# Optimization experiments

Measured on AMD Instinct MI355X. Metric: run time of the kernel, lower is better.

Reference implementation:

```python
import jax, jax.numpy as jnp
import numpy as np

H = 64  # hidden_size
IN = 1  # input_size
OUT = 32  # fc output


def _lstm_layer(x, Wih, Whh, bih, bhh):
    """x: (B,T,D_in). Returns (outputs (B,T,H), final h (B,H)). PyTorch gate order i,f,g,o."""
    B = x.shape[0]
    b = bih + bhh  # (4H,)
    # precompute input contributions for all timesteps: (T,B,4H)
    xW = jnp.einsum('btd,gd->tbg', x, Wih) + b

    def step(carry, xw_t):
        h, c = carry
        gates = xw_t + h @ Whh.T  # (B,4H)
        i, f, g, o = jnp.split(gates, 4, axis=-1)
        i = jax.nn.sigmoid(i)
        f = jax.nn.sigmoid(f)
        g = jnp.tanh(g)
        o = jax.nn.sigmoid(o)
        c = f * c + i * g
        h = o * jnp.tanh(c)
        return (h, c), h

    h0 = jnp.zeros((B, H), dtype=x.dtype)
    c0 = jnp.zeros((B, H), dtype=x.dtype)
    (h_T, _), hs = jax.lax.scan(step, (h0, c0), xW)
    return jnp.swapaxes(hs, 0, 1), h_T


def setup_inputs() -> dict:
    key = jax.random.key(0)
    ks = jax.random.split(key, 11)
    s_ih0 = 1.0 / np.sqrt(H)
    inp = {
        'x': jax.random.normal(ks[0], (2048, 512, IN), dtype=jnp.float32),
        # layer 0: input_size -> H
        'Wih0': jax.random.uniform(ks[1], (4 * H, IN), minval=-s_ih0, maxval=s_ih0),
        'Whh0': jax.random.uniform(ks[2], (4 * H, H), minval=-s_ih0, maxval=s_ih0),
        'bih0': jax.random.uniform(ks[3], (4 * H,), minval=-s_ih0, maxval=s_ih0),
        'bhh0': jax.random.uniform(ks[4], (4 * H,), minval=-s_ih0, maxval=s_ih0),
        # layer 1: H -> H
        'Wih1': jax.random.uniform(ks[5], (4 * H, H), minval=-s_ih0, maxval=s_ih0),
        'Whh1': jax.random.uniform(ks[6], (4 * H, H), minval=-s_ih0, maxval=s_ih0),
        'bih1': jax.random.uniform(ks[7], (4 * H,), minval=-s_ih0, maxval=s_ih0),
        'bhh1': jax.random.uniform(ks[8], (4 * H,), minval=-s_ih0, maxval=s_ih0),
        # fc: H -> 32
        'fcW': jax.random.uniform(ks[9], (OUT, H), minval=-s_ih0, maxval=s_ih0),
        'fcb': jax.random.uniform(ks[10], (OUT,), minval=-s_ih0, maxval=s_ih0),
    }
    return inp


def reference(x, Wih0, Whh0, bih0, bhh0, Wih1, Whh1, bih1, bhh1, fcW, fcb):
    h1_seq, _ = _lstm_layer(x, Wih0, Whh0, bih0, bhh0)
    _, h_last = _lstm_layer(h1_seq, Wih1, Whh1, bih1, bhh1)  # hidden[-1]
    features = jax.nn.relu(h_last @ fcW.T + fcb)  # (B, 32)
    return features
```

## Files before the change

kernel.cpp:

```cpp
#include <hip/hip_runtime.h>
#include <hip/hip_bf16.h>


#define HID 64
#define TSTEPS 512
#define MB 8
#define RS 80

typedef _Float16 f16x8 __attribute__((ext_vector_type(8)));
typedef float f32x4 __attribute__((ext_vector_type(4)));

#define KSIG (-1.44269504089f)
#define KTANH (2.88539008178f)

__device__ __forceinline__ float fsig(float x) {
    return __builtin_amdgcn_rcpf(1.f + __builtin_amdgcn_exp2f(KSIG * x));
}
__device__ __forceinline__ float ftanh(float x) {
    return 1.f - 2.f * __builtin_amdgcn_rcpf(1.f + __builtin_amdgcn_exp2f(KTANH * x));
}

__global__ __launch_bounds__(512, 1) void lstm_feat_kernel(
    const float* __restrict__ x,
    const float* __restrict__ Wih0, const float* __restrict__ Whh0,
    const float* __restrict__ bih0, const float* __restrict__ bhh0,
    const float* __restrict__ Wih1, const float* __restrict__ Whh1,
    const float* __restrict__ bih1, const float* __restrict__ bhh1,
    const float* __restrict__ fcW, const float* __restrict__ fcb,
    float* __restrict__ out)
{
    __shared__ float x_lds[TSTEPS * MB];
    __shared__ __align__(16) _Float16 h0_lds[2][MB * RS];
    __shared__ __align__(16) _Float16 h1_lds[2][MB * RS];
    __shared__ float h1f32[MB * HID];
    __shared__ float fcw_lds[HID * 32];
    __shared__ float fcb_lds[32];

    const int tid  = threadIdx.x;
    const int wave = tid >> 6;
    const int lane = tid & 63;
    const int nq   = lane & 15;
    const int quad = lane >> 4;
    const int bbase = blockIdx.x * MB;
    const bool isL1 = (wave >= 4);
    const int ug = wave & 3;
    const int u  = ug * 16 + nq;

    for (int i = tid; i < TSTEPS * MB; i += 512) {
        int r = i >> 9, t = i & (TSTEPS - 1);
        x_lds[t * MB + r] = x[(bbase + r) * TSTEPS + t];
    }
    for (int i = tid; i < 32 * HID; i += 512) {
        int o = i >> 6, kk = i & 63;
        fcw_lds[kk * 32 + o] = fcW[i];
    }
    if (tid < 32) fcb_lds[tid] = fcb[tid];
    for (int i = tid; i < 2 * MB * RS; i += 512) {
        ((_Float16*)h0_lds)[i] = (_Float16)0.f;
        ((_Float16*)h1_lds)[i] = (_Float16)0.f;
    }

    f16x8 wA[4][2], wB[4][2];
    float bA[4], wx0[4];
    {
        const float* Wa = isL1 ? Wih1 : Whh0;
        const float* Wb = isL1 ? Whh1 : Whh0;
        const float* bi = isL1 ? bih1 : bih0;
        const float* bh = isL1 ? bhh1 : bhh0;
        #pragma unroll
        for (int g = 0; g < 4; ++g) {
            const int n = g * 64 + u;
            bA[g]  = bi[n] + bh[n];
            wx0[g] = Wih0[n];
            #pragma unroll
            for (int ks = 0; ks < 2; ++ks) {
                const int k0 = quad * 8 + ks * 32;
                f16x8 a, b;
                #pragma unroll
                for (int j = 0; j < 8; ++j) {
                    a[j] = (_Float16)Wa[n * HID + k0 + j];
                    b[j] = (_Float16)Wb[n * HID + k0 + j];
                }
                wA[g][ks] = a; wB[g][ks] = b;
            }
        }
    }

    const f32x4 zero4 = {0.f, 0.f, 0.f, 0.f};
    const int arow = (nq >> 1) * RS + quad * 8;
    const int b0 = quad * 2;
    float c0 = 0.f, c1 = 0.f;

    __syncthreads();

    int p = 0;
    for (int k = 0; k < TSTEPS; ++k) {
        const int q = p ^ 1;
        if (!isL1) {
            f16x8 a0[2];
            a0[0] = *(const f16x8*)&h0_lds[p][arow];
            a0[1] = *(const f16x8*)&h0_lds[p][arow + 32];
            const float2 xq = *(const float2*)&x_lds[k * MB + b0];
            f32x4 acc[4];
            #pragma unroll
            for (int g = 0; g < 4; ++g)
                acc[g] = __builtin_amdgcn_mfma_f32_16x16x32_f16(a0[0], wA[g][0], zero4, 0, 0, 0);
            #pragma unroll
            for (int g = 0; g < 4; ++g)
                acc[g] = __builtin_amdgcn_mfma_f32_16x16x32_f16(a0[1], wA[g][1], acc[g], 0, 0, 0);
            {
                const float pi = acc[0][0] + fmaf(xq.x, wx0[0], bA[0]);
                const float pf = acc[1][0] + fmaf(xq.x, wx0[1], bA[1]);
                const float pg = acc[2][0] + fmaf(xq.x, wx0[2], bA[2]);
                const float po = acc[3][0] + fmaf(xq.x, wx0[3], bA[3]);
                const float iv = fsig(pi), fv = fsig(pf), gv = ftanh(pg), ov = fsig(po);
                c0 = fv * c0 + iv * gv;
                h0_lds[q][b0 * RS + u] = (_Float16)(ov * ftanh(c0));
            }
            {
                const float pi = acc[0][2] + fmaf(xq.y, wx0[0], bA[0]);
                const float pf = acc[1][2] + fmaf(xq.y, wx0[1], bA[1]);
                const float pg = acc[2][2] + fmaf(xq.y, wx0[2], bA[2]);
                const float po = acc[3][2] + fmaf(xq.y, wx0[3], bA[3]);
                const float iv = fsig(pi), fv = fsig(pf), gv = ftanh(pg), ov = fsig(po);
                c1 = fv * c1 + iv * gv;
                h0_lds[q][(b0 + 1) * RS + u] = (_Float16)(ov * ftanh(c1));
            }
        } else {
            f16x8 a0[2], a1[2];
            a0[0] = *(const f16x8*)&h0_lds[p][arow];
            a0[1] = *(const f16x8*)&h0_lds[p][arow + 32];
            a1[0] = *(const f16x8*)&h1_lds[p][arow];
            a1[1] = *(const f16x8*)&h1_lds[p][arow + 32];
            f32x4 accA[4], accB[4];
            #pragma unroll
            for (int g = 0; g < 4; ++g)
                accA[g] = __builtin_amdgcn_mfma_f32_16x16x32_f16(a0[0], wA[g][0], zero4, 0, 0, 0);
            #pragma unroll
            for (int g = 0; g < 4; ++g)
                accB[g] = __builtin_amdgcn_mfma_f32_16x16x32_f16(a1[0], wB[g][0], zero4, 0, 0, 0);
            #pragma unroll
            for (int g = 0; g < 4; ++g)
                accA[g] = __builtin_amdgcn_mfma_f32_16x16x32_f16(a0[1], wA[g][1], accA[g], 0, 0, 0);
            #pragma unroll
            for (int g = 0; g < 4; ++g)
                accB[g] = __builtin_amdgcn_mfma_f32_16x16x32_f16(a1[1], wB[g][1], accB[g], 0, 0, 0);
            if (k > 0) {
                {
                    const float pi = accA[0][0] + accB[0][0] + bA[0];
                    const float pf = accA[1][0] + accB[1][0] + bA[1];
                    const float pg = accA[2][0] + accB[2][0] + bA[2];
                    const float po = accA[3][0] + accB[3][0] + bA[3];
                    const float iv = fsig(pi), fv = fsig(pf), gv = ftanh(pg), ov = fsig(po);
                    c0 = fv * c0 + iv * gv;
                    h1_lds[q][b0 * RS + u] = (_Float16)(ov * ftanh(c0));
                }
                {
                    const float pi = accA[0][2] + accB[0][2] + bA[0];
                    const float pf = accA[1][2] + accB[1][2] + bA[1];
                    const float pg = accA[2][2] + accB[2][2] + bA[2];
                    const float po = accA[3][2] + accB[3][2] + bA[3];
                    const float iv = fsig(pi), fv = fsig(pf), gv = ftanh(pg), ov = fsig(po);
                    c1 = fv * c1 + iv * gv;
                    h1_lds[q][(b0 + 1) * RS + u] = (_Float16)(ov * ftanh(c1));
                }
            }
        }
        p = q;
        __syncthreads();
    }

    if (isL1) {
        f16x8 a0[2], a1[2];
        a0[0] = *(const f16x8*)&h0_lds[p][arow];
        a0[1] = *(const f16x8*)&h0_lds[p][arow + 32];
        a1[0] = *(const f16x8*)&h1_lds[p][arow];
        a1[1] = *(const f16x8*)&h1_lds[p][arow + 32];
        f32x4 accA[4], accB[4];
        #pragma unroll
        for (int g = 0; g < 4; ++g)
            accA[g] = __builtin_amdgcn_mfma_f32_16x16x32_f16(a0[0], wA[g][0], zero4, 0, 0, 0);
        #pragma unroll
        for (int g = 0; g < 4; ++g)
            accB[g] = __builtin_amdgcn_mfma_f32_16x16x32_f16(a1[0], wB[g][0], zero4, 0, 0, 0);
        #pragma unroll
        for (int g = 0; g < 4; ++g)
            accA[g] = __builtin_amdgcn_mfma_f32_16x16x32_f16(a0[1], wA[g][1], accA[g], 0, 0, 0);
        #pragma unroll
        for (int g = 0; g < 4; ++g)
            accB[g] = __builtin_amdgcn_mfma_f32_16x16x32_f16(a1[1], wB[g][1], accB[g], 0, 0, 0);
        {
            const float pi = accA[0][0] + accB[0][0] + bA[0];
            const float pf = accA[1][0] + accB[1][0] + bA[1];
            const float pg = accA[2][0] + accB[2][0] + bA[2];
            const float po = accA[3][0] + accB[3][0] + bA[3];
            const float iv = fsig(pi), fv = fsig(pf), gv = ftanh(pg), ov = fsig(po);
            c0 = fv * c0 + iv * gv;
            h1f32[b0 * HID + u] = ov * ftanh(c0);
        }
        {
            const float pi = accA[0][2] + accB[0][2] + bA[0];
            const float pf = accA[1][2] + accB[1][2] + bA[1];
            const float pg = accA[2][2] + accB[2][2] + bA[2];
            const float po = accA[3][2] + accB[3][2] + bA[3];
            const float iv = fsig(pi), fv = fsig(pf), gv = ftanh(pg), ov = fsig(po);
            c1 = fv * c1 + iv * gv;
            h1f32[(b0 + 1) * HID + u] = ov * ftanh(c1);
        }
    }
    __syncthreads();

    if (tid < MB * 32) {
        const int o  = tid & 31;
        const int rr = tid >> 5;
        float acc = fcb_lds[o];
        #pragma unroll 8
        for (int kk = 0; kk < HID; ++kk)
            acc += h1f32[rr * HID + kk] * fcw_lds[kk * 32 + o];
        out[(bbase + rr) * 32 + o] = fmaxf(acc, 0.f);
    }
}

extern "C" void kernel_launch(void* const* d_in, const int* in_sizes, int n_in,
                              void* d_out, int out_size, void* d_ws, size_t ws_size,
                              hipStream_t stream) {
    const float* x    = (const float*)d_in[0];
    const float* Wih0 = (const float*)d_in[1];
    const float* Whh0 = (const float*)d_in[2];
    const float* bih0 = (const float*)d_in[3];
    const float* bhh0 = (const float*)d_in[4];
    const float* Wih1 = (const float*)d_in[5];
    const float* Whh1 = (const float*)d_in[6];
    const float* bih1 = (const float*)d_in[7];
    const float* bhh1 = (const float*)d_in[8];
    const float* fcW  = (const float*)d_in[9];
    const float* fcb  = (const float*)d_in[10];
    float* out = (float*)d_out;

    lstm_feat_kernel<<<2048 / MB, 512, 0, stream>>>(
        x, Wih0, Whh0, bih0, bhh0, Wih1, Whh1, bih1, bhh1, fcW, fcb, out);
}
```

Measured before the change: 358.4 us.

## Fold activation scales and bias into MFMA, pack gate math as float2

Pre-scales the weights, biases and input weights by the sigmoid and tanh exp2 constants, so the activations skip a multiply. The bias now seeds the MFMA accumulator instead of being added afterwards. The two batch rows' gate math is written as float2 vectors so the compiler can emit packed FP32 ops. The loop is unrolled by two with fixed buffer indices, x is re-laid out for one 16-byte load per pair of steps, and s_setprio is raised around the MFMA burst. Scaling weights before the fp16 conversion slightly changes rounding.

Result: faster. 316.0 us (-11.8%).

```diff
diff --git a/kernel.cpp b/kernel.cpp
--- a/kernel.cpp
+++ b/kernel.cpp
@@ -9,16 +9,20 @@
 
 typedef _Float16 f16x8 __attribute__((ext_vector_type(8)));
 typedef float f32x4 __attribute__((ext_vector_type(4)));
+typedef float f32x2 __attribute__((ext_vector_type(2)));
 
 #define KSIG (-1.44269504089f)
 #define KTANH (2.88539008178f)
 
-__device__ __forceinline__ float fsig(float x) {
-    return __builtin_amdgcn_rcpf(1.f + __builtin_amdgcn_exp2f(KSIG * x));
-}
-__device__ __forceinline__ float ftanh(float x) {
-    return 1.f - 2.f * __builtin_amdgcn_rcpf(1.f + __builtin_amdgcn_exp2f(KTANH * x));
-}
+__device__ __forceinline__ f32x2 mk2(float a, float b) { f32x2 r; r[0] = a; r[1] = b; return r; }
+__device__ __forceinline__ f32x2 exp2v(f32x2 v) {
+    f32x2 r; r[0] = __builtin_amdgcn_exp2f(v[0]); r[1] = __builtin_amdgcn_exp2f(v[1]); return r;
+}
+__device__ __forceinline__ f32x2 rcpv(f32x2 v) {
+    f32x2 r; r[0] = __builtin_amdgcn_rcpf(v[0]); r[1] = __builtin_amdgcn_rcpf(v[1]); return r;
+}
+__device__ __forceinline__ f32x2 sig2(f32x2 p)  { return rcpv(exp2v(p) + 1.0f); }
+__device__ __forceinline__ f32x2 tanh2(f32x2 p) { return 1.0f - 2.0f * rcpv(exp2v(p) + 1.0f); }
 
 __global__ __launch_bounds__(512, 1) void lstm_feat_kernel(
     const float* __restrict__ x,
@@ -29,7 +33,7 @@
     const float* __restrict__ fcW, const float* __restrict__ fcb,
     float* __restrict__ out)
 {
-    __shared__ float x_lds[TSTEPS * MB];
+    __shared__ float x_lds[(MB / 2) * TSTEPS * 2];
     __shared__ __align__(16) _Float16 h0_lds[2][MB * RS];
     __shared__ __align__(16) _Float16 h1_lds[2][MB * RS];
     __shared__ float h1f32[MB * HID];
@@ -48,7 +52,7 @@
 
     for (int i = tid; i < TSTEPS * MB; i += 512) {
         int r = i >> 9, t = i & (TSTEPS - 1);
-        x_lds[t * MB + r] = x[(bbase + r) * TSTEPS + t];
+        x_lds[(r >> 1) * (TSTEPS * 2) + t * 2 + (r & 1)] = x[(bbase + r) * TSTEPS + t];
     }
     for (int i = tid; i < 32 * HID; i += 512) {
         int o = i >> 6, kk = i & 63;
@@ -61,7 +65,8 @@
     }
 
     f16x8 wA[4][2], wB[4][2];
-    float bA[4], wx0[4];
+    f32x4 cbias[4];
+    float wx0s[4];
     {
         const float* Wa = isL1 ? Wih1 : Whh0;
         const float* Wb = isL1 ? Whh1 : Whh0;
@@ -69,17 +74,19 @@
         const float* bh = isL1 ? bhh1 : bhh0;
         #pragma unroll
         for (int g = 0; g < 4; ++g) {
+            const float sc = (g == 2) ? KTANH : KSIG;
             const int n = g * 64 + u;
-            bA[g]  = bi[n] + bh[n];
-            wx0[g] = Wih0[n];
+            const float bs = (bi[n] + bh[n]) * sc;
+            cbias[g] = (f32x4){bs, bs, bs, bs};
+            wx0s[g] = Wih0[n] * sc;
             #pragma unroll
             for (int ks = 0; ks < 2; ++ks) {
                 const int k0 = quad * 8 + ks * 32;
                 f16x8 a, b;
                 #pragma unroll
                 for (int j = 0; j < 8; ++j) {
-                    a[j] = (_Float16)Wa[n * HID + k0 + j];
-                    b[j] = (_Float16)Wb[n * HID + k0 + j];
+                    a[j] = (_Float16)(Wa[n * HID + k0 + j] * sc);
+                    b[j] = (_Float16)(Wb[n * HID + k0 + j] * sc);
                 }
                 wA[g][ks] = a; wB[g][ks] = b;
             }
@@ -88,125 +95,114 @@
 
     const f32x4 zero4 = {0.f, 0.f, 0.f, 0.f};
     const int arow = (nq >> 1) * RS + quad * 8;
-    const int b0 = quad * 2;
-    float c0 = 0.f, c1 = 0.f;
+    const int b0r  = (quad * 2) * RS;
+    const int hbase = quad * 2;
+    f32x2 cc = mk2(0.f, 0.f);
 
     __syncthreads();
 
-    int p = 0;
-    for (int k = 0; k < TSTEPS; ++k) {
-        const int q = p ^ 1;
+#define L0_SUB(P, Q, XQ2) do {                                                       \
+    f16x8 a0_ = *(const f16x8*)&h0_lds[P][arow];                                     \
+    f16x8 a1_ = *(const f16x8*)&h0_lds[P][arow + 32];                                \
+    f32x4 ac[4];                                                                     \
+    __builtin_amdgcn_s_setprio(1);                                                   \
+    _Pragma("unroll")                                                                \
+    for (int g = 0; g < 4; ++g)                                                      \
+        ac[g] = __builtin_amdgcn_mfma_f32_16x16x32_f16(a0_, wA[g][0], cbias[g], 0, 0, 0); \
+    _Pragma("unroll")                                                                \
+    for (int g = 0; g < 4; ++g)                                                      \
+        ac[g] = __builtin_amdgcn_mfma_f32_16x16x32_f16(a1_, wA[g][1], ac[g], 0, 0, 0); \
+    __builtin_amdgcn_s_setprio(0);                                                   \
+    f32x2 pi = (XQ2) * wx0s[0] + mk2(ac[0][0], ac[0][2]);                            \
+    f32x2 pf = (XQ2) * wx0s[1] + mk2(ac[1][0], ac[1][2]);                            \
+    f32x2 pg = (XQ2) * wx0s[2] + mk2(ac[2][0], ac[2][2]);                            \
+    f32x2 po = (XQ2) * wx0s[3] + mk2(ac[3][0], ac[3][2]);                            \
+    f32x2 iv = sig2(pi), fv = sig2(pf), gv = tanh2(pg), ov = sig2(po);               \
+    cc = fv * cc + iv * gv;                                                          \
+    f32x2 hh = ov * tanh2(cc * KTANH);                                               \
+    h0_lds[Q][b0r + u]      = (_Float16)hh[0];                                       \
+    h0_lds[Q][b0r + RS + u] = (_Float16)hh[1];                                       \
+} while (0)
+
+#define L1_SUB(P, Q, GUARD) do {                                                     \
+    f16x8 a00 = *(const f16x8*)&h0_lds[P][arow];                                     \
+    f16x8 a01 = *(const f16x8*)&h0_lds[P][arow + 32];                                \
+    f16x8 a10 = *(const f16x8*)&h1_lds[P][arow];                                     \
+    f16x8 a11 = *(const f16x8*)&h1_lds[P][arow + 32];                                \
+    f32x4 aA[4], aB[4];                                                              \
+    __builtin_amdgcn_s_setprio(1);                                                   \
+    _Pragma("unroll")                                                                \
+    for (int g = 0; g < 4; ++g)                                                      \
+        aA[g] = __builtin_amdgcn_mfma_f32_16x16x32_f16(a00, wA[g][0], zero4, 0, 0, 0); \
+    _Pragma("unroll")                                                                \
+    for (int g = 0; g < 4; ++g)                                                      \
+        aB[g] = __builtin_amdgcn_mfma_f32_16x16x32_f16(a10, wB[g][0], cbias[g], 0, 0, 0); \
+    _Pragma("unroll")                                                                \
+    for (int g = 0; g < 4; ++g)                                                      \
+        aA[g] = __builtin_amdgcn_mfma_f32_16x16x32_f16(a01, wA[g][1], aA[g], 0, 0, 0); \
+    _Pragma("unroll")                                                                \
+    for (int g = 0; g < 4; ++g)                                                      \
+        aB[g] = __builtin_amdgcn_mfma_f32_16x16x32_f16(a11, wB[g][1], aB[g], 0, 0, 0); \
+    __builtin_amdgcn_s_setprio(0);                                                   \
+    if (GUARD) {                                                                     \
+        f32x2 pi = mk2(aA[0][0], aA[0][2]) + mk2(aB[0][0], aB[0][2]);                \
+        f32x2 pf = mk2(aA[1][0], aA[1][2]) + mk2(aB[1][0], aB[1][2]);                \
+        f32x2 pg = mk2(aA[2][0], aA[2][2]) + mk2(aB[2][0], aB[2][2]);                \
+        f32x2 po = mk2(aA[3][0], aA[3][2]) + mk2(aB[3][0], aB[3][2]);                \
+        f32x2 iv = sig2(pi), fv = sig2(pf), gv = tanh2(pg), ov = sig2(po);           \
+        cc = fv * cc + iv * gv;                                                      \
+        f32x2 hh = ov * tanh2(cc * KTANH);                                           \
+        h1_lds[Q][b0r + u]      = (_Float16)hh[0];                                   \
+        h1_lds[Q][b0r + RS + u] = (_Float16)hh[1];                                   \
+    }                                                                                \
+} while (0)
+
+    const int xoff = quad * (TSTEPS * 2);
+    for (int k = 0; k < TSTEPS; k += 2) {
+        f32x2 xa, xb;
         if (!isL1) {
-            f16x8 a0[2];
-            a0[0] = *(const f16x8*)&h0_lds[p][arow];
-            a0[1] = *(const f16x8*)&h0_lds[p][arow + 32];
-            const float2 xq = *(const float2*)&x_lds[k * MB + b0];
-            f32x4 acc[4];
-            #pragma unroll
-            for (int g = 0; g < 4; ++g)
-                acc[g] = __builtin_amdgcn_mfma_f32_16x16x32_f16(a0[0], wA[g][0], zero4, 0, 0, 0);
-            #pragma unroll
-            for (int g = 0; g < 4; ++g)
-                acc[g] = __builtin_amdgcn_mfma_f32_16x16x32_f16(a0[1], wA[g][1], acc[g], 0, 0, 0);
-            {
-                const float pi = acc[0][0] + fmaf(xq.x, wx0[0], bA[0]);
-                const float pf = acc[1][0] + fmaf(xq.x, wx0[1], bA[1]);
-                const float pg = acc[2][0] + fmaf(xq.x, wx0[2], bA[2]);
-                const float po = acc[3][0] + fmaf(xq.x, wx0[3], bA[3]);
-                const float iv = fsig(pi), fv = fsig(pf), gv = ftanh(pg), ov = fsig(po);
-                c0 = fv * c0 + iv * gv;
-                h0_lds[q][b0 * RS + u] = (_Float16)(ov * ftanh(c0));
-            }
-            {
-                const float pi = acc[0][2] + fmaf(xq.y, wx0[0], bA[0]);
-                const float pf = acc[1][2] + fmaf(xq.y, wx0[1], bA[1]);
-                const float pg = acc[2][2] + fmaf(xq.y, wx0[2], bA[2]);
-                const float po = acc[3][2] + fmaf(xq.y, wx0[3], bA[3]);
-                const float iv = fsig(pi), fv = fsig(pf), gv = ftanh(pg), ov = fsig(po);
-                c1 = fv * c1 + iv * gv;
-                h0_lds[q][(b0 + 1) * RS + u] = (_Float16)(ov * ftanh(c1));
-            }
+            const f32x4 xv = *(const f32x4*)&x_lds[xoff + k * 2];
+            xa = mk2(xv[0], xv[1]); xb = mk2(xv[2], xv[3]);
+            L0_SUB(0, 1, xa);
         } else {
-            f16x8 a0[2], a1[2];
-            a0[0] = *(const f16x8*)&h0_lds[p][arow];
-            a0[1] = *(const f16x8*)&h0_lds[p][arow + 32];
-            a1[0] = *(const f16x8*)&h1_lds[p][arow];
-            a1[1] = *(const f16x8*)&h1_lds[p][arow + 32];
-            f32x4 accA[4], accB[4];
-            #pragma unroll
-            for (int g = 0; g < 4; ++g)
-                accA[g] = __builtin_amdgcn_mfma_f32_16x16x32_f16(a0[0], wA[g][0], zero4, 0, 0, 0);
-            #pragma unroll
-            for (int g = 0; g < 4; ++g)
-                accB[g] = __builtin_amdgcn_mfma_f32_16x16x32_f16(a1[0], wB[g][0], zero4, 0, 0, 0);
-            #pragma unroll
-            for (int g = 0; g < 4; ++g)
-                accA[g] = __builtin_amdgcn_mfma_f32_16x16x32_f16(a0[1], wA[g][1], accA[g], 0, 0, 0);
-            #pragma unroll
-            for (int g = 0; g < 4; ++g)
-                accB[g] = __builtin_amdgcn_mfma_f32_16x16x32_f16(a1[1], wB[g][1], accB[g], 0, 0, 0);
-            if (k > 0) {
-                {
-                    const float pi = accA[0][0] + accB[0][0] + bA[0];
-                    const float pf = accA[1][0] + accB[1][0] + bA[1];
-                    const float pg = accA[2][0] + accB[2][0] + bA[2];
-                    const float po = accA[3][0] + accB[3][0] + bA[3];
-                    const float iv = fsig(pi), fv = fsig(pf), gv = ftanh(pg), ov = fsig(po);
-                    c0 = fv * c0 + iv * gv;
-                    h1_lds[q][b0 * RS + u] = (_Float16)(ov * ftanh(c0));
-                }
-                {
-                    const float pi = accA[0][2] + accB[0][2] + bA[0];
-                    const float pf = accA[1][2] + accB[1][2] + bA[1];
-                    const float pg = accA[2][2] + accB[2][2] + bA[2];
-                    const float po = accA[3][2] + accB[3][2] + bA[3];
-                    const float iv = fsig(pi), fv = fsig(pf), gv = ftanh(pg), ov = fsig(po);
-                    c1 = fv * c1 + iv * gv;
-                    h1_lds[q][(b0 + 1) * RS + u] = (_Float16)(ov * ftanh(c1));
-                }
-            }
+            L1_SUB(0, 1, (k > 0));
         }
-        p = q;
         __syncthreads();
+        if (!isL1) {
+            L0_SUB(1, 0, xb);
+        } else {
+            L1_SUB(1, 0, true);
+        }
+        __syncthreads();
     }
 
     if (isL1) {
-        f16x8 a0[2], a1[2];
-        a0[0] = *(const f16x8*)&h0_lds[p][arow];
-        a0[1] = *(const f16x8*)&h0_lds[p][arow + 32];
-        a1[0] = *(const f16x8*)&h1_lds[p][arow];
-        a1[1] = *(const f16x8*)&h1_lds[p][arow + 32];
-        f32x4 accA[4], accB[4];
-        #pragma unroll
-        for (int g = 0; g < 4; ++g)
-            accA[g] = __builtin_amdgcn_mfma_f32_16x16x32_f16(a0[0], wA[g][0], zero4, 0, 0, 0);
-        #pragma unroll
-        for (int g = 0; g < 4; ++g)
-            accB[g] = __builtin_amdgcn_mfma_f32_16x16x32_f16(a1[0], wB[g][0], zero4, 0, 0, 0);
-        #pragma unroll
-        for (int g = 0; g < 4; ++g)
-            accA[g] = __builtin_amdgcn_mfma_f32_16x16x32_f16(a0[1], wA[g][1], accA[g], 0, 0, 0);
-        #pragma unroll
-        for (int g = 0; g < 4; ++g)
-            accB[g] = __builtin_amdgcn_mfma_f32_16x16x32_f16(a1[1], wB[g][1], accB[g], 0, 0, 0);
-        {
-            const float pi = accA[0][0] + accB[0][0] + bA[0];
-            const float pf = accA[1][0] + accB[1][0] + bA[1];
-            const float pg = accA[2][0] + accB[2][0] + bA[2];
-            const float po = accA[3][0] + accB[3][0] + bA[3];
-            const float iv = fsig(pi), fv = fsig(pf), gv = ftanh(pg), ov = fsig(po);
-            c0 = fv * c0 + iv * gv;
-            h1f32[b0 * HID + u] = ov * ftanh(c0);
-        }
-        {
-            const float pi = accA[0][2] + accB[0][2] + bA[0];
-            const float pf = accA[1][2] + accB[1][2] + bA[1];
-            const float pg = accA[2][2] + accB[2][2] + bA[2];
-            const float po = accA[3][2] + accB[3][2] + bA[3];
-            const float iv = fsig(pi), fv = fsig(pf), gv = ftanh(pg), ov = fsig(po);
-            c1 = fv * c1 + iv * gv;
-            h1f32[(b0 + 1) * HID + u] = ov * ftanh(c1);
-        }
+        f16x8 a00 = *(const f16x8*)&h0_lds[0][arow];
+        f16x8 a01 = *(const f16x8*)&h0_lds[0][arow + 32];
+        f16x8 a10 = *(const f16x8*)&h1_lds[0][arow];
+        f16x8 a11 = *(const f16x8*)&h1_lds[0][arow + 32];
+        f32x4 aA[4], aB[4];
+        #pragma unroll
+        for (int g = 0; g < 4; ++g)
+            aA[g] = __builtin_amdgcn_mfma_f32_16x16x32_f16(a00, wA[g][0], zero4, 0, 0, 0);
+        #pragma unroll
+        for (int g = 0; g < 4; ++g)
+            aB[g] = __builtin_amdgcn_mfma_f32_16x16x32_f16(a10, wB[g][0], cbias[g], 0, 0, 0);
+        #pragma unroll
+        for (int g = 0; g < 4; ++g)
+            aA[g] = __builtin_amdgcn_mfma_f32_16x16x32_f16(a01, wA[g][1], aA[g], 0, 0, 0);
+        #pragma unroll
+        for (int g = 0; g < 4; ++g)
+            aB[g] = __builtin_amdgcn_mfma_f32_16x16x32_f16(a11, wB[g][1], aB[g], 0, 0, 0);
+        f32x2 pi = mk2(aA[0][0], aA[0][2]) + mk2(aB[0][0], aB[0][2]);
+        f32x2 pf = mk2(aA[1][0], aA[1][2]) + mk2(aB[1][0], aB[1][2]);
+        f32x2 pg = mk2(aA[2][0], aA[2][2]) + mk2(aB[2][0], aB[2][2]);
+        f32x2 po = mk2(aA[3][0], aA[3][2]) + mk2(aB[3][0], aB[3][2]);
+        f32x2 iv = sig2(pi), fv = sig2(pf), gv = tanh2(pg), ov = sig2(po);
+        cc = fv * cc + iv * gv;
+        f32x2 hh = ov * tanh2(cc * KTANH);
+        h1f32[hbase * HID + u]       = hh[0];
+        h1f32[(hbase + 1) * HID + u] = hh[1];
     }
     __syncthreads();
 
```
